# Kernel optimization log

Measured on AMD Instinct MI355X. Metric: run time of the kernel, lower is better.

The kernel has to match this reference:

```python
import jax, jax.numpy as jnp
import numpy as np

N_POINTS = 16384
N_GAUSS = 3200
N_CLASSES = 14
BOX = 10.0  # scene half-extent


def setup_inputs() -> dict:
    key = jax.random.key(0)
    ks = jax.random.split(key, 6)
    xyz = jax.random.uniform(ks[0], (N_POINTS, 3), jnp.float32, -BOX, BOX)
    means = jax.random.uniform(ks[1], (N_GAUSS, 3), jnp.float32, -BOX, BOX)
    scales = jax.random.uniform(ks[2], (N_GAUSS, 3), jnp.float32, 0.5, 2.0)
    rotations = jax.random.normal(ks[3], (N_GAUSS, 4), jnp.float32)
    opacities = jax.random.uniform(ks[4], (N_GAUSS,), jnp.float32, 0.1, 1.0)
    semantics = jax.random.normal(ks[5], (N_GAUSS, N_CLASSES), jnp.float32)
    return {"xyz": xyz, "means": means, "scales": scales,
            "rotations": rotations, "opacities": opacities, "semantics": semantics}


def quat_to_rot(q):
    # q: [G,4] in (w, x, y, z) order, normalized first (matches torch helper)
    q = q / jnp.linalg.norm(q, axis=-1, keepdims=True)
    w, x, y, z = q[:, 0], q[:, 1], q[:, 2], q[:, 3]
    R = jnp.stack([
        1 - 2 * (y * y + z * z), 2 * (x * y - w * z),     2 * (x * z + w * y),
        2 * (x * y + w * z),     1 - 2 * (x * x + z * z), 2 * (y * z - w * x),
        2 * (x * z - w * y),     2 * (y * z + w * x),     1 - 2 * (x * x + y * y),
    ], axis=-1).reshape(-1, 3, 3)
    return R


def reference(xyz, means, scales, rotations, opacities, semantics):
    # Cov = (S R)^T (S R) = R^T diag(s^2) R ; closed-form inverse (R orthonormal):
    # CovInv = R^T diag(1/s^2) R  -- fused analytic 3x3 inverse.
    R = quat_to_rot(rotations)                      # [G,3,3]
    inv_var = 1.0 / (scales * scales)               # [G,3]
    CovInv = jnp.einsum('gki,gk,gkj->gij', R, inv_var, R)  # [G,3,3]

    # Quadratic form q[n,g] = (x_n - mu_g)^T A_g (x_n - mu_g), expanded so that
    # only [N,G] is materialized (no [N,G,3] intermediates):
    Amu = jnp.einsum('gij,gj->gi', CovInv, means)   # [G,3]
    muAmu = jnp.sum(means * Amu, axis=-1)           # [G]
    P = (xyz[:, :, None] * xyz[:, None, :]).reshape(-1, 9)   # [N,9]
    Aflat = CovInv.reshape(-1, 9)                   # [G,9]
    q = P @ Aflat.T - 2.0 * (xyz @ Amu.T) + muAmu[None, :]   # [N,G]

    # Gaussian splat aggregation: semantics weighted by opacity * Gaussian kernel
    w = opacities[None, :] * jnp.exp(-0.5 * q)      # [N,G]
    out = w @ semantics                              # [N,C]
    return out
```

## Files before the change

kernel.cpp:

```cpp
#include <hip/hip_runtime.h>
#include <hip/hip_bf16.h>

#define N_POINTS 16384
#define N_GAUSS  3200
#define N_CLASSES 14
#define NCHUNK (N_GAUSS / 32)

typedef _Float16 half8  __attribute__((ext_vector_type(8)));
typedef float    f32x4  __attribute__((ext_vector_type(4)));

#define WS_CREC_OFF 0
#define WS_SEMP_OFF 204800

__global__ void gauss_prep_kernel(const float* __restrict__ means,
                                  const float* __restrict__ scales,
                                  const float* __restrict__ rotations,
                                  const float* __restrict__ opacities,
                                  const float* __restrict__ semantics,
                                  _Float16* __restrict__ crec,
                                  _Float16* __restrict__ semP) {
    const int g = blockIdx.x * blockDim.x + threadIdx.x;
    if (g >= N_GAUSS) return;

    float qw = rotations[g * 4 + 0];
    float qx = rotations[g * 4 + 1];
    float qy = rotations[g * 4 + 2];
    float qz = rotations[g * 4 + 3];
    float inv = 1.0f / sqrtf(qw * qw + qx * qx + qy * qy + qz * qz);
    qw *= inv; qx *= inv; qy *= inv; qz *= inv;

    float r00 = 1.0f - 2.0f * (qy * qy + qz * qz);
    float r01 = 2.0f * (qx * qy - qw * qz);
    float r02 = 2.0f * (qx * qz + qw * qy);
    float r10 = 2.0f * (qx * qy + qw * qz);
    float r11 = 1.0f - 2.0f * (qx * qx + qz * qz);
    float r12 = 2.0f * (qy * qz - qw * qx);
    float r20 = 2.0f * (qx * qz - qw * qy);
    float r21 = 2.0f * (qy * qz + qw * qx);
    float r22 = 1.0f - 2.0f * (qx * qx + qy * qy);

    float sx = scales[g * 3 + 0];
    float sy = scales[g * 3 + 1];
    float sz = scales[g * 3 + 2];
    float iv0 = 1.0f / (sx * sx);
    float iv1 = 1.0f / (sy * sy);
    float iv2 = 1.0f / (sz * sz);

    float a00 = iv0 * r00 * r00 + iv1 * r10 * r10 + iv2 * r20 * r20;
    float a01 = iv0 * r00 * r01 + iv1 * r10 * r11 + iv2 * r20 * r21;
    float a02 = iv0 * r00 * r02 + iv1 * r10 * r12 + iv2 * r20 * r22;
    float a11 = iv0 * r01 * r01 + iv1 * r11 * r11 + iv2 * r21 * r21;
    float a12 = iv0 * r01 * r02 + iv1 * r11 * r12 + iv2 * r21 * r22;
    float a22 = iv0 * r02 * r02 + iv1 * r12 * r12 + iv2 * r22 * r22;

    float mx = means[g * 3 + 0];
    float my = means[g * 3 + 1];
    float mz = means[g * 3 + 2];
    float amx = a00 * mx + a01 * my + a02 * mz;
    float amy = a01 * mx + a11 * my + a12 * mz;
    float amz = a02 * mx + a12 * my + a22 * mz;
    float muAmu = mx * amx + my * amy + mz * amz;

    const float k = -0.72134752044448170368f;

    float C[10];
    C[0] = k * a00;  C[1] = k * a11;  C[2] = k * a22;
    C[3] = 2.0f * k * a01;  C[4] = 2.0f * k * a02;  C[5] = 2.0f * k * a12;
    C[6] = -2.0f * k * amx; C[7] = -2.0f * k * amy; C[8] = -2.0f * k * amz;
    C[9] = k * muAmu + log2f(opacities[g]);

    _Float16* rec = crec + (size_t)g * 32;
#pragma unroll
    for (int kk = 0; kk < 10; ++kk) {
        _Float16 h = (_Float16)C[kk];
        rec[kk]      = h;
        rec[10 + kk] = (_Float16)(C[kk] - (float)h);
        rec[20 + kk] = h;
    }
    rec[30] = (_Float16)0; rec[31] = (_Float16)0;

    const int cidx = g >> 5, r = g & 31;
    const int gt = r >> 4, grpW = (r >> 2) & 3, i = r & 3;
    const int p = grpW * 8 + gt * 4 + i;
#pragma unroll
    for (int c = 0; c < N_CLASSES; ++c)
        semP[(size_t)c * N_GAUSS + cidx * 32 + p] = (_Float16)semantics[g * N_CLASSES + c];
}

__launch_bounds__(1024, 4)
__global__ void gauss_occ_main_kernel(const float* __restrict__ xyz,
                                      const _Float16* __restrict__ crec,
                                      const _Float16* __restrict__ semP,
                                      float* __restrict__ out) {
    __shared__ unsigned int wbuf[16][64][16];

    const int tid  = threadIdx.x;
    const int lane = tid & 63;
    const int wid  = __builtin_amdgcn_readfirstlane(tid >> 6);
    const int pg   = blockIdx.x;

    const int c0 = 6 * wid + (wid >= 4) + (wid >= 7) + (wid >= 10) + (wid >= 13);
    const int cnt = 6 + ((wid == 3) | (wid == 6) | (wid == 9) | (wid == 12));
    const int c1 = c0 + cnt;

    const int m   = lane & 15;
    const int mm  = (m < N_CLASSES) ? m : (N_CLASSES - 1);
    const int grp = lane >> 4;
    const int frs = (m >> 1) & 3;
    const int wsz = (lane >> 1) & 3;

    const int pt = pg * 64 + lane;
    const float x = xyz[pt * 3 + 0];
    const float y = xyz[pt * 3 + 1];
    const float z = xyz[pt * 3 + 2];

    unsigned int (*wrow)[16] = wbuf[wid];

    {
        float P[10] = {x * x, y * y, z * z, x * y, x * z, y * z, x, y, z, 1.0f};
        _Float16 Ph[10], Pl[10];
#pragma unroll
        for (int j = 0; j < 10; ++j) {
            Ph[j] = (_Float16)P[j];
            Pl[j] = (_Float16)(P[j] - (float)Ph[j]);
        }
        half8 b0, b1, b2, b3;
#pragma unroll
        for (int j = 0; j < 8; ++j) b0[j] = Ph[j];
        b1[0] = Ph[8]; b1[1] = Ph[9];
#pragma unroll
        for (int j = 0; j < 6; ++j) b1[2 + j] = Ph[j];
#pragma unroll
        for (int j = 0; j < 4; ++j) { b2[j] = Ph[6 + j]; b2[4 + j] = Pl[j]; }
#pragma unroll
        for (int j = 0; j < 6; ++j) b3[j] = Pl[4 + j];
        b3[6] = (_Float16)0; b3[7] = (_Float16)0;
        *(half8*)&wrow[lane][(0 ^ wsz) * 4] = b0;
        *(half8*)&wrow[lane][(1 ^ wsz) * 4] = b1;
        *(half8*)&wrow[lane][(2 ^ wsz) * 4] = b2;
        *(half8*)&wrow[lane][(3 ^ wsz) * 4] = b3;
    }

    half8 f1[4];
#pragma unroll
    for (int s = 0; s < 4; ++s)
        f1[s] = *(const half8*)&wrow[s * 16 + m][(grp ^ frs) * 4];

    f32x4 acc0 = {0.f, 0.f, 0.f, 0.f};
    f32x4 acc1 = {0.f, 0.f, 0.f, 0.f};
    f32x4 acc2 = {0.f, 0.f, 0.f, 0.f};
    f32x4 acc3 = {0.f, 0.f, 0.f, 0.f};
    const f32x4 z4 = {0.f, 0.f, 0.f, 0.f};

    const _Float16* pA = crec + ((size_t)(c0 * 32 + m)) * 32 + grp * 8;
    const _Float16* pB = semP + (size_t)mm * N_GAUSS + c0 * 32 + grp * 8;
    half8 A0 = *(const half8*)pA;
    half8 A1 = *(const half8*)(pA + 512);
    half8 bS = *(const half8*)pB;

    for (int c = c0; c < c1; ++c) {
        pA += 1024;
        pB += 32;
        const half8 nA0 = *(const half8*)pA;
        const half8 nA1 = *(const half8*)(pA + 512);
        const half8 nbS = *(const half8*)pB;

#pragma unroll
        for (int s = 0; s < 4; ++s) {
            f32x4 t0 = __builtin_amdgcn_mfma_f32_16x16x32_f16(A0, f1[s], z4, 0, 0, 0);
            f32x4 t1 = __builtin_amdgcn_mfma_f32_16x16x32_f16(A1, f1[s], z4, 0, 0, 0);

            const float e0 = __builtin_amdgcn_exp2f(t0[0]);
            const float e1 = __builtin_amdgcn_exp2f(t0[1]);
            const float e2 = __builtin_amdgcn_exp2f(t0[2]);
            const float e3 = __builtin_amdgcn_exp2f(t0[3]);
            const float e4 = __builtin_amdgcn_exp2f(t1[0]);
            const float e5 = __builtin_amdgcn_exp2f(t1[1]);
            const float e6 = __builtin_amdgcn_exp2f(t1[2]);
            const float e7 = __builtin_amdgcn_exp2f(t1[3]);

            *(uint4*)&wrow[s * 16 + m][(grp ^ frs) * 4] = make_uint4(
                __builtin_bit_cast(unsigned int, __builtin_amdgcn_cvt_pkrtz(e0, e1)),
                __builtin_bit_cast(unsigned int, __builtin_amdgcn_cvt_pkrtz(e2, e3)),
                __builtin_bit_cast(unsigned int, __builtin_amdgcn_cvt_pkrtz(e4, e5)),
                __builtin_bit_cast(unsigned int, __builtin_amdgcn_cvt_pkrtz(e6, e7)));
        }

        const half8 a0 = *(const half8*)&wrow[ 0 + m][(grp ^ frs) * 4];
        const half8 a1 = *(const half8*)&wrow[16 + m][(grp ^ frs) * 4];
        const half8 a2 = *(const half8*)&wrow[32 + m][(grp ^ frs) * 4];
        const half8 a3 = *(const half8*)&wrow[48 + m][(grp ^ frs) * 4];
        acc0 = __builtin_amdgcn_mfma_f32_16x16x32_f16(a0, bS, acc0, 0, 0, 0);
        acc1 = __builtin_amdgcn_mfma_f32_16x16x32_f16(a1, bS, acc1, 0, 0, 0);
        acc2 = __builtin_amdgcn_mfma_f32_16x16x32_f16(a2, bS, acc2, 0, 0, 0);
        acc3 = __builtin_amdgcn_mfma_f32_16x16x32_f16(a3, bS, acc3, 0, 0, 0);

        A0 = nA0; A1 = nA1; bS = nbS;
    }

    float* red = (float*)&wbuf[0][0][0];
#pragma unroll
    for (int i = 0; i < 4; ++i) {
        red[wid * 1024 + ( 0 + grp * 4 + i) * 16 + m] = acc0[i];
        red[wid * 1024 + (16 + grp * 4 + i) * 16 + m] = acc1[i];
        red[wid * 1024 + (32 + grp * 4 + i) * 16 + m] = acc2[i];
        red[wid * 1024 + (48 + grp * 4 + i) * 16 + m] = acc3[i];
    }
    __syncthreads();

    if (tid < 64 * N_CLASSES) {
        const int l = tid / N_CLASSES;
        const int cc = tid - l * N_CLASSES;
        float s = 0.0f;
#pragma unroll
        for (int wq = 0; wq < 16; ++wq) s += red[wq * 1024 + l * 16 + cc];
        out[(size_t)pg * (64 * N_CLASSES) + tid] = s;
    }
}

extern "C" void kernel_launch(void* const* d_in, const int* in_sizes, int n_in,
                              void* d_out, int out_size, void* d_ws, size_t ws_size,
                              hipStream_t stream) {
    const float* xyz       = (const float*)d_in[0];
    const float* means     = (const float*)d_in[1];
    const float* scales    = (const float*)d_in[2];
    const float* rotations = (const float*)d_in[3];
    const float* opacities = (const float*)d_in[4];
    const float* semantics = (const float*)d_in[5];
    float* out = (float*)d_out;

    _Float16* crec = (_Float16*)((char*)d_ws + WS_CREC_OFF);
    _Float16* semP = (_Float16*)((char*)d_ws + WS_SEMP_OFF);

    hipLaunchKernelGGL(gauss_prep_kernel,
                       dim3(50), dim3(64), 0, stream,
                       means, scales, rotations, opacities, semantics, crec, semP);

    hipLaunchKernelGGL(gauss_occ_main_kernel,
                       dim3(256), dim3(1024), 0, stream,
                       xyz, crec, semP, out);
}
```

Before: 18.65 us.

## Double-buffer the LDS weight tile to overlap exp phase with PV MFMA

Splits each wave's LDS weight buffer into two halves and software-pipelines the loop. The quadratic-form MFMA, exp and store for chunk c+1 now run while the semantic-accumulation MFMAs read chunk c from the other buffer. The aim is to break the write-then-read dependency on a single LDS tile so MFMA and transcendental work can interleave. In exchange, LDS use doubles to 128KB per block, which may limit occupancy, and the loop needs a prologue and epilogue.

New measurement: 19.26 us. 1.03x slower.

```diff
diff --git a/kernel.cpp b/kernel.cpp
--- a/kernel.cpp
+++ b/kernel.cpp
@@ -92,7 +92,7 @@
                                       const _Float16* __restrict__ crec,
                                       const _Float16* __restrict__ semP,
                                       float* __restrict__ out) {
-    __shared__ unsigned int wbuf[16][64][16];
+    __shared__ unsigned int wbuf[16][2][64][16];
 
     const int tid  = threadIdx.x;
     const int lane = tid & 63;
@@ -114,7 +114,8 @@
     const float y = xyz[pt * 3 + 1];
     const float z = xyz[pt * 3 + 2];
 
-    unsigned int (*wrow)[16] = wbuf[wid];
+    unsigned int (*bufA)[16] = wbuf[wid][0];
+    unsigned int (*bufB)[16] = wbuf[wid][1];
 
     {
         float P[10] = {x * x, y * y, z * z, x * y, x * z, y * z, x, y, z, 1.0f};
@@ -135,16 +136,16 @@
 #pragma unroll
         for (int j = 0; j < 6; ++j) b3[j] = Pl[4 + j];
         b3[6] = (_Float16)0; b3[7] = (_Float16)0;
-        *(half8*)&wrow[lane][(0 ^ wsz) * 4] = b0;
-        *(half8*)&wrow[lane][(1 ^ wsz) * 4] = b1;
-        *(half8*)&wrow[lane][(2 ^ wsz) * 4] = b2;
-        *(half8*)&wrow[lane][(3 ^ wsz) * 4] = b3;
+        *(half8*)&bufA[lane][(0 ^ wsz) * 4] = b0;
+        *(half8*)&bufA[lane][(1 ^ wsz) * 4] = b1;
+        *(half8*)&bufA[lane][(2 ^ wsz) * 4] = b2;
+        *(half8*)&bufA[lane][(3 ^ wsz) * 4] = b3;
     }
 
     half8 f1[4];
 #pragma unroll
     for (int s = 0; s < 4; ++s)
-        f1[s] = *(const half8*)&wrow[s * 16 + m][(grp ^ frs) * 4];
+        f1[s] = *(const half8*)&bufA[s * 16 + m][(grp ^ frs) * 4];
 
     f32x4 acc0 = {0.f, 0.f, 0.f, 0.f};
     f32x4 acc1 = {0.f, 0.f, 0.f, 0.f};
@@ -152,59 +153,80 @@
     f32x4 acc3 = {0.f, 0.f, 0.f, 0.f};
     const f32x4 z4 = {0.f, 0.f, 0.f, 0.f};
 
+#define QPH(BUF, QA0, QA1)                                                     \
+    {                                                                          \
+        _Pragma("unroll")                                                      \
+        for (int s = 0; s < 4; ++s) {                                          \
+            f32x4 t0 = __builtin_amdgcn_mfma_f32_16x16x32_f16(QA0, f1[s], z4, 0, 0, 0); \
+            f32x4 t1 = __builtin_amdgcn_mfma_f32_16x16x32_f16(QA1, f1[s], z4, 0, 0, 0); \
+            const float e0 = __builtin_amdgcn_exp2f(t0[0]);                    \
+            const float e1 = __builtin_amdgcn_exp2f(t0[1]);                    \
+            const float e2 = __builtin_amdgcn_exp2f(t0[2]);                    \
+            const float e3 = __builtin_amdgcn_exp2f(t0[3]);                    \
+            const float e4 = __builtin_amdgcn_exp2f(t1[0]);                    \
+            const float e5 = __builtin_amdgcn_exp2f(t1[1]);                    \
+            const float e6 = __builtin_amdgcn_exp2f(t1[2]);                    \
+            const float e7 = __builtin_amdgcn_exp2f(t1[3]);                    \
+            *(uint4*)&BUF[s * 16 + m][(grp ^ frs) * 4] = make_uint4(           \
+                __builtin_bit_cast(unsigned int, __builtin_amdgcn_cvt_pkrtz(e0, e1)), \
+                __builtin_bit_cast(unsigned int, __builtin_amdgcn_cvt_pkrtz(e2, e3)), \
+                __builtin_bit_cast(unsigned int, __builtin_amdgcn_cvt_pkrtz(e4, e5)), \
+                __builtin_bit_cast(unsigned int, __builtin_amdgcn_cvt_pkrtz(e6, e7))); \
+        }                                                                      \
+    }
+
+#define PVH(BUF, BSEM)                                                         \
+    {                                                                          \
+        const half8 a0 = *(const half8*)&BUF[ 0 + m][(grp ^ frs) * 4];         \
+        const half8 a1 = *(const half8*)&BUF[16 + m][(grp ^ frs) * 4];         \
+        const half8 a2 = *(const half8*)&BUF[32 + m][(grp ^ frs) * 4];         \
+        const half8 a3 = *(const half8*)&BUF[48 + m][(grp ^ frs) * 4];         \
+        acc0 = __builtin_amdgcn_mfma_f32_16x16x32_f16(a0, BSEM, acc0, 0, 0, 0);\
+        acc1 = __builtin_amdgcn_mfma_f32_16x16x32_f16(a1, BSEM, acc1, 0, 0, 0);\
+        acc2 = __builtin_amdgcn_mfma_f32_16x16x32_f16(a2, BSEM, acc2, 0, 0, 0);\
+        acc3 = __builtin_amdgcn_mfma_f32_16x16x32_f16(a3, BSEM, acc3, 0, 0, 0);\
+    }
+
     const _Float16* pA = crec + ((size_t)(c0 * 32 + m)) * 32 + grp * 8;
     const _Float16* pB = semP + (size_t)mm * N_GAUSS + c0 * 32 + grp * 8;
-    half8 A0 = *(const half8*)pA;
-    half8 A1 = *(const half8*)(pA + 512);
-    half8 bS = *(const half8*)pB;
-
-    for (int c = c0; c < c1; ++c) {
-        pA += 1024;
-        pB += 32;
-        const half8 nA0 = *(const half8*)pA;
-        const half8 nA1 = *(const half8*)(pA + 512);
-        const half8 nbS = *(const half8*)pB;
-
-#pragma unroll
-        for (int s = 0; s < 4; ++s) {
-            f32x4 t0 = __builtin_amdgcn_mfma_f32_16x16x32_f16(A0, f1[s], z4, 0, 0, 0);
-            f32x4 t1 = __builtin_amdgcn_mfma_f32_16x16x32_f16(A1, f1[s], z4, 0, 0, 0);
-
-            const float e0 = __builtin_amdgcn_exp2f(t0[0]);
-            const float e1 = __builtin_amdgcn_exp2f(t0[1]);
-            const float e2 = __builtin_amdgcn_exp2f(t0[2]);
-            const float e3 = __builtin_amdgcn_exp2f(t0[3]);
-            const float e4 = __builtin_amdgcn_exp2f(t1[0]);
-            const float e5 = __builtin_amdgcn_exp2f(t1[1]);
-            const float e6 = __builtin_amdgcn_exp2f(t1[2]);
-            const float e7 = __builtin_amdgcn_exp2f(t1[3]);
-
-            *(uint4*)&wrow[s * 16 + m][(grp ^ frs) * 4] = make_uint4(
-                __builtin_bit_cast(unsigned int, __builtin_amdgcn_cvt_pkrtz(e0, e1)),
-                __builtin_bit_cast(unsigned int, __builtin_amdgcn_cvt_pkrtz(e2, e3)),
-                __builtin_bit_cast(unsigned int, __builtin_amdgcn_cvt_pkrtz(e4, e5)),
-                __builtin_bit_cast(unsigned int, __builtin_amdgcn_cvt_pkrtz(e6, e7)));
-        }
-
-        const half8 a0 = *(const half8*)&wrow[ 0 + m][(grp ^ frs) * 4];
-        const half8 a1 = *(const half8*)&wrow[16 + m][(grp ^ frs) * 4];
-        const half8 a2 = *(const half8*)&wrow[32 + m][(grp ^ frs) * 4];
-        const half8 a3 = *(const half8*)&wrow[48 + m][(grp ^ frs) * 4];
-        acc0 = __builtin_amdgcn_mfma_f32_16x16x32_f16(a0, bS, acc0, 0, 0, 0);
-        acc1 = __builtin_amdgcn_mfma_f32_16x16x32_f16(a1, bS, acc1, 0, 0, 0);
-        acc2 = __builtin_amdgcn_mfma_f32_16x16x32_f16(a2, bS, acc2, 0, 0, 0);
-        acc3 = __builtin_amdgcn_mfma_f32_16x16x32_f16(a3, bS, acc3, 0, 0, 0);
-
-        A0 = nA0; A1 = nA1; bS = nbS;
-    }
-
-    float* red = (float*)&wbuf[0][0][0];
+    {
+        const half8 qA0 = *(const half8*)pA;
+        const half8 qA1 = *(const half8*)(pA + 512);
+        QPH(bufA, qA0, qA1);
+    }
+    half8 pvB = *(const half8*)pB;
+    pA += 1024; pB += 32;
+    half8 nqA0 = *(const half8*)pA;
+    half8 nqA1 = *(const half8*)(pA + 512);
+    half8 npvB = *(const half8*)pB;
+
+    unsigned int (*bufQ)[16] = bufB;
+    unsigned int (*bufP)[16] = bufA;
+
+    for (int c = c0; c < c1 - 1; ++c) {
+        pA += 1024; pB += 32;
+        const half8 fA0 = *(const half8*)pA;
+        const half8 fA1 = *(const half8*)(pA + 512);
+        const half8 fB  = *(const half8*)pB;
+
+        QPH(bufQ, nqA0, nqA1);
+        PVH(bufP, pvB);
+
+        pvB = npvB;
+        nqA0 = fA0; nqA1 = fA1; npvB = fB;
+        unsigned int (*t)[16] = bufQ; bufQ = bufP; bufP = t;
+    }
+    PVH(bufP, pvB);
+#undef QPH
+#undef PVH
+
+    float* red = (float*)&wbuf[0][0][0][0];
 #pragma unroll
     for (int i = 0; i < 4; ++i) {
-        red[wid * 1024 + ( 0 + grp * 4 + i) * 16 + m] = acc0[i];
-        red[wid * 1024 + (16 + grp * 4 + i) * 16 + m] = acc1[i];
-        red[wid * 1024 + (32 + grp * 4 + i) * 16 + m] = acc2[i];
-        red[wid * 1024 + (48 + grp * 4 + i) * 16 + m] = acc3[i];
+        red[wid * 2048 + ( 0 + grp * 4 + i) * 16 + m] = acc0[i];
+        red[wid * 2048 + (16 + grp * 4 + i) * 16 + m] = acc1[i];
+        red[wid * 2048 + (32 + grp * 4 + i) * 16 + m] = acc2[i];
+        red[wid * 2048 + (48 + grp * 4 + i) * 16 + m] = acc3[i];
     }
     __syncthreads();
 
@@ -213,7 +235,7 @@
         const int cc = tid - l * N_CLASSES;
         float s = 0.0f;
 #pragma unroll
-        for (int wq = 0; wq < 16; ++wq) s += red[wq * 1024 + l * 16 + cc];
+        for (int wq = 0; wq < 16; ++wq) s += red[wq * 2048 + l * 16 + cc];
         out[(size_t)pg * (64 * N_CLASSES) + tid] = s;
     }
 }
```
